# Performance work log

Hardware: AMD Instinct MI355X
Metric: run time of the kernel (lower is better)

## Reference

```python
import jax, jax.numpy as jnp
import numpy as np

B, S, D, H = 4, 127, 768, 12
HD = D // H
NS = S + 1
GAMMA = 1.0
NEG_INF = -1e9
EPS = 1e-6


def setup_inputs() -> dict:
    key = jax.random.key(0)
    ks = jax.random.split(key, 12)
    s = 0.02
    return {
        'desc': jax.random.normal(ks[0], (B, S, D), jnp.float32),
        'nve': jax.random.normal(ks[1], (B, NS, D), jnp.float32),
        'mask_M': jax.random.uniform(ks[2], (B, H, S, S), jnp.float32),
        'Wq': jax.random.normal(ks[3], (D, D), jnp.float32) * s,
        'bq': jnp.zeros((D,), jnp.float32),
        'Wk': jax.random.normal(ks[4], (D, D), jnp.float32) * s,
        'bk': jnp.zeros((D,), jnp.float32),
        'Wv': jax.random.normal(ks[5], (D, D), jnp.float32) * s,
        'bv': jnp.zeros((D,), jnp.float32),
        'eW1': jax.random.normal(ks[6], (2 * D, D), jnp.float32) * s,
        'eb1': jnp.zeros((D,), jnp.float32),
        'ln_g': jnp.ones((D,), jnp.float32),
        'ln_b': jnp.zeros((D,), jnp.float32),
        'eW2': jax.random.normal(ks[7], (D, D), jnp.float32) * s,
        'eb2': jnp.zeros((D,), jnp.float32),
        'aW': jax.random.normal(ks[8], (3 * HD,), jnp.float32) * s,
        'ab': jnp.zeros((), jnp.float32),
    }


def _layernorm(x, g, b):
    m = jnp.mean(x, -1, keepdims=True)
    v = jnp.var(x, -1, keepdims=True)
    return (x - m) * jax.lax.rsqrt(v + 1e-5) * g + b


def _adjacency():
    # CLS->Var on, Var->CLS off, Var-Var without self loop
    var_adj = 1.0 - jnp.eye(S, dtype=jnp.float32)
    adj = jnp.zeros((NS, NS), jnp.float32)
    adj = adj.at[1:, 1:].set(var_adj)
    adj = adj.at[0, 1:].set(1.0)
    return adj  # [NS, NS]


def reference(desc, nve, mask_M, Wq, bq, Wk, bk, Wv, bv, eW1, eb1, ln_g, ln_b, eW2, eb2, aW, ab):
    adj = _adjacency()

    def proj(W, bias):
        return (nve @ W + bias).reshape(B, NS, H, HD).transpose(0, 2, 1, 3)  # [B,H,NS,HD]

    q, k, v = proj(Wq, bq), proj(Wk, bk), proj(Wv, bv)

    # edge features: pairwise concat of desc embeddings, CLS edges = [desc, desc]
    node_i = jnp.broadcast_to(desc[:, :, None, :], (B, S, S, D))
    node_j = jnp.broadcast_to(desc[:, None, :, :], (B, S, S, D))
    var_edge = jnp.concatenate([node_i, node_j], -1)           # [B,S,S,2D]
    cls_edge = jnp.concatenate([desc, desc], -1)               # [B,S,2D]
    edge = jnp.zeros((B, NS, NS, 2 * D), jnp.float32)
    edge = edge.at[:, 1:, 1:].set(var_edge)
    edge = edge.at[:, 0, 1:].set(cls_edge)
    edge = edge.at[:, 1:, 0].set(cls_edge)

    # edge_update MLP: Linear -> LayerNorm -> ReLU -> Linear
    h = jax.nn.relu(_layernorm(edge @ eW1 + eb1, ln_g, ln_b))
    e = h @ eW2 + eb2                                           # [B,NS,NS,D]
    e = e.reshape(B, NS, NS, H, HD).transpose(0, 3, 1, 2, 4)    # [B,H,NS,NS,HD]
    e = e * adj[None, None, :, :, None]

    # attn_proj on concat([q_i, k_j, e_ij]) == sum of three dot products + bias
    aq, ak, ae = aW[:HD], aW[HD:2 * HD], aW[2 * HD:]
    logits = (jnp.einsum('bhid,d->bhi', q, aq)[:, :, :, None]
              + jnp.einsum('bhjd,d->bhj', k, ak)[:, :, None, :]
              + jnp.einsum('bhijd,d->bhij', e, ae) + ab)        # [B,H,NS,NS]

    # logit bias from Var-Var probabilities
    p = jnp.clip(mask_M, EPS, 1.0 - EPS)
    bias = (jnp.log(p) - jnp.log(1.0 - p)) * GAMMA
    logits = logits.at[:, :, 1:, 1:].add(bias)

    logits = logits + jnp.where(adj == 0.0, NEG_INF, 0.0)[None, None]
    attn = jax.nn.softmax(logits, axis=-1)                      # dropout off (eval)
    context = jnp.einsum('bhij,bhjd->bhid', attn, v)
    basis_outputs = context.transpose(0, 2, 1, 3)               # [B,NS,H,HD]
    return basis_outputs, attn
```

## Files before the change

### kernel.cpp

```cpp
#include <hip/hip_runtime.h>
#include <hip/hip_bf16.h>

#define BB  4
#define SS  127
#define DD  768
#define HH  12
#define HDl 64
#define NSl 128

typedef __attribute__((ext_vector_type(8))) short short8;
typedef __attribute__((ext_vector_type(4))) float f32x4;

constexpr int OFF_P   = 0;
constexpr int OFF_Q   = OFF_P  + BB*SS*DD;
constexpr int OFF_V   = OFF_Q  + BB*SS*DD;
constexpr int OFF_QA  = OFF_V  + BB*NSl*DD;
constexpr int OFF_KA  = OFF_QA + BB*NSl*HH;
constexpr int OFF_W2B = OFF_KA + BB*NSl*HH;
constexpr int OFF_WQA = OFF_W2B + 6144;
constexpr int OFF_WKA = OFF_WQA + HH*DD;
constexpr int OFF_BF  = OFF_WKA + HH*DD;
constexpr int OFF_SP  = OFF_BF + 64;
constexpr int OFF_SSP = OFF_SP + BB*128;
constexpr int OFF_SQ  = OFF_SSP + BB*128;
constexpr int OFF_SSQ = OFF_SQ + BB*128;
constexpr int OFF_EL  = OFF_SSQ + BB*128;

__device__ inline unsigned short f2bf(float f) {
    unsigned int u = __builtin_bit_cast(unsigned int, f);
    u += 0x7fffu + ((u >> 16) & 1u);
    return (unsigned short)(u >> 16);
}

__device__ inline short8 pack8(float4 a, float4 b) {
    short8 p;
    p[0] = (short)f2bf(a.x); p[1] = (short)f2bf(a.y);
    p[2] = (short)f2bf(a.z); p[3] = (short)f2bf(a.w);
    p[4] = (short)f2bf(b.x); p[5] = (short)f2bf(b.y);
    p[6] = (short)f2bf(b.z); p[7] = (short)f2bf(b.w);
    return p;
}

__device__ inline void unpack8(short8 s, float* f) {
    int4 u = __builtin_bit_cast(int4, s);
    f[0] = __builtin_bit_cast(float, u.x << 16);
    f[1] = __builtin_bit_cast(float, u.x & 0xffff0000);
    f[2] = __builtin_bit_cast(float, u.y << 16);
    f[3] = __builtin_bit_cast(float, u.y & 0xffff0000);
    f[4] = __builtin_bit_cast(float, u.z << 16);
    f[5] = __builtin_bit_cast(float, u.z & 0xffff0000);
    f[6] = __builtin_bit_cast(float, u.w << 16);
    f[7] = __builtin_bit_cast(float, u.w & 0xffff0000);
}

__device__ inline unsigned int cvtpk(float lo, float hi) {
    unsigned int r;
    asm volatile("v_cvt_pk_bf16_f32 %0, %1, %2" : "=v"(r) : "v"(lo), "v"(hi));
    return r;
}

constexpr int NB_PQ   = 96;
constexpr int NB_V    = 96;
constexpr int FOLD_T  = 3 * HH * DD + 36 + 4 * DD;
constexpr int NB_FOLD = (FOLD_T + 511) / 512;

__global__ __launch_bounds__(512) void mega1(
        const float* __restrict__ desc, const float* __restrict__ nve,
        const float* __restrict__ eW1, const float* __restrict__ Wv,
        const float* __restrict__ bv, const float* __restrict__ eb1,
        const float* __restrict__ Wq, const float* __restrict__ Wk,
        const float* __restrict__ eW2,
        const float* __restrict__ bq, const float* __restrict__ bk,
        const float* __restrict__ eb2, const float* __restrict__ aW,
        float* __restrict__ P, float* __restrict__ Qm, float* __restrict__ V,
        unsigned short* __restrict__ W2Bu, float* __restrict__ WQA,
        float* __restrict__ WKA, float* __restrict__ bfold) {
    const int bid = blockIdx.x;
    const int tid = threadIdx.x;

    if (bid >= NB_PQ + NB_V) {
        int idx = (bid - NB_PQ - NB_V) * 512 + tid;
        const int total = 3 * HH * DD;
        if (idx < total) {
            int which = idx / (HH * DD);
            int r = idx % (HH * DD);
            int h = r / DD;
            int c = r % DD;
            const float* W = (which == 0) ? eW2 : (which == 1) ? Wq : Wk;
            const float* a = (which == 0) ? (aW + 2 * HDl) : (which == 1) ? aW : (aW + HDl);
            float s = 0.f;
            #pragma unroll 8
            for (int d = 0; d < HDl; ++d) s += W[c * DD + h * HDl + d] * a[d];
            if (which == 0) W2Bu[h * DD + c] = f2bf(s);
            else if (which == 1) WQA[h * DD + c] = s;
            else WKA[h * DD + c] = s;
        } else if (idx < total + 36) {
            int r = idx - total;
            int which = r / HH, h = r % HH;
            const float* bb = (which == 0) ? eb2 : (which == 1) ? bq : bk;
            const float* a = (which == 0) ? (aW + 2 * HDl) : (which == 1) ? aW : (aW + HDl);
            float s = 0.f;
            for (int d = 0; d < HDl; ++d) s += bb[h * HDl + d] * a[d];
            bfold[r] = s;
        } else if (idx < FOLD_T) {
            W2Bu[12 * DD + (idx - total - 36)] = 0;
        }
        return;
    }

    const bool pq = (bid < NB_PQ);
    const int r = pq ? bid : bid - NB_PQ;
    const int bcol = (r % 12) * 64;
    const int brow = (r / 12) * 64;
    const float* A  = pq ? desc : nve;
    const float* B0 = pq ? eW1 : Wv;
    const int M = pq ? (BB * SS) : (BB * NSl);

    __shared__ short lds[3 * 64 * 64];
    short* As  = lds;
    short* Bs0 = lds + 4096;
    short* Bs1 = lds + 8192;

    const int arow = tid >> 3, akc = (tid & 7) * 8;
    const int abyte = (arow * 128 + akc * 2) ^ ((arow & 7) << 4);
    const int bn = tid & 63, bg = tid >> 6;
    const int bbyte = (bn * 128 + bg * 16) ^ ((bn & 7) << 4);

    const int gm = brow + arow;
    const float* arow_p = A + gm * DD + akc;

    short8 gA, gB0, gB1;
    auto loadA = [&](int k0) {
        float4 f0 = {0,0,0,0}, f1 = {0,0,0,0};
        if (gm < M) {
            f0 = *(const float4*)(arow_p + k0);
            f1 = *(const float4*)(arow_p + k0 + 4);
        }
        gA = pack8(f0, f1);
    };
    auto loadB = [&](const float* Bm, int k0, short8& dst) {
        float v[8];
        #pragma unroll
        for (int q = 0; q < 8; ++q)
            v[q] = Bm[(k0 + bg * 8 + q) * DD + bcol + bn];
        short8 p;
        #pragma unroll
        for (int q = 0; q < 8; ++q) p[q] = (short)f2bf(v[q]);
        dst = p;
    };

    loadA(0);
    loadB(B0, 0, gB0);
    if (pq) loadB(eW1 + DD * DD, 0, gB1);

    const int lane = tid & 63;
    const int w = tid >> 6;
    const int wr = w >> 1, wc = w & 1;
    const int l15 = lane & 15;

    f32x4 acc0[2] = {};
    f32x4 acc1[2] = {};

    for (int k0 = 0; k0 < DD; k0 += 64) {
        *(short8*)((char*)As + abyte) = gA;
        *(short8*)((char*)Bs0 + bbyte) = gB0;
        if (pq) *(short8*)((char*)Bs1 + bbyte) = gB1;
        __syncthreads();
        if (k0 + 64 < DD) {
            loadA(k0 + 64);
            loadB(B0, k0 + 64, gB0);
            if (pq) loadB(eW1 + DD * DD, k0 + 64, gB1);
        }
        #pragma unroll
        for (int ks = 0; ks < 2; ++ks) {
            const int kb = ks * 64 + ((lane >> 4) << 4);
            int row = wr * 16 + l15;
            short8 af = *(const short8*)((char*)As + ((row * 128 + kb) ^ ((row & 7) << 4)));
            #pragma unroll
            for (int ni = 0; ni < 2; ++ni) {
                int col = wc * 32 + ni * 16 + l15;
                int cb = (col * 128 + kb) ^ ((col & 7) << 4);
                short8 b0 = *(const short8*)((char*)Bs0 + cb);
                acc0[ni] = __builtin_amdgcn_mfma_f32_16x16x32_bf16(af, b0, acc0[ni], 0, 0, 0);
                if (pq) {
                    short8 b1 = *(const short8*)((char*)Bs1 + cb);
                    acc1[ni] = __builtin_amdgcn_mfma_f32_16x16x32_bf16(af, b1, acc1[ni], 0, 0, 0);
                }
            }
        }
        __syncthreads();
    }

    #pragma unroll
    for (int ni = 0; ni < 2; ++ni) {
        int gcol = bcol + wc * 32 + ni * 16 + l15;
        float bias0 = pq ? 0.f : bv[gcol];
        float bias1 = pq ? eb1[gcol] : 0.f;
        #pragma unroll
        for (int rr = 0; rr < 4; ++rr) {
            int grow = brow + wr * 16 + ((lane >> 4) << 2) + rr;
            if (grow < M) {
                if (pq) {
                    P[grow * DD + gcol]  = acc0[ni][rr];
                    Qm[grow * DD + gcol] = acc1[ni][rr] + bias1;
                } else {
                    V[grow * DD + gcol] = acc0[ni][rr] + bias0;
                }
            }
        }
    }
}

__global__ void statqk_kernel(const float* __restrict__ Pp, const float* __restrict__ Qp,
                              const float* __restrict__ nve,
                              const float* __restrict__ WQA, const float* __restrict__ WKA,
                              const float* __restrict__ bfold,
                              float* __restrict__ SP, float* __restrict__ SSP,
                              float* __restrict__ SQ, float* __restrict__ SSQ,
                              float* __restrict__ qa, float* __restrict__ ka) {
    int wid = blockIdx.x * 4 + (threadIdx.x >> 6);
    int lane = threadIdx.x & 63;
    const int NSTAT = BB * SS * 2;
    if (wid < NSTAT) {
        int which = wid & 1;
        int row = (wid >> 1) % SS;
        int b = (wid >> 1) / SS;
        const float* src = (which ? Qp : Pp) + (b * SS + row) * DD;
        float s = 0.f, ss = 0.f;
        #pragma unroll
        for (int r = 0; r < 12; ++r) {
            float v = src[lane + 64 * r];
            s += v;
            ss += v * v;
        }
        #pragma unroll
        for (int off = 32; off; off >>= 1) {
            s += __shfl_xor(s, off);
            ss += __shfl_xor(ss, off);
        }
        if (lane == 0) {
            (which ? SQ : SP)[b * 128 + row] = s;
            (which ? SSQ : SSP)[b * 128 + row] = ss;
        }
    } else {
        int t2 = wid - NSTAT;
        if (t2 >= BB * NSl * HH * 2) return;
        int which = t2 & 1;
        int r = t2 >> 1;
        int h = r % HH;
        int t = (r / HH) % NSl;
        int b = r / (HH * NSl);
        const float* W = (which ? WKA : WQA) + h * DD;
        const float* row = nve + (b * NSl + t) * DD;
        float s = 0.f;
        #pragma unroll
        for (int rr = 0; rr < 12; ++rr) {
            int c = lane + 64 * rr;
            s += row[c] * W[c];
        }
        #pragma unroll
        for (int off = 32; off; off >>= 1) s += __shfl_xor(s, off);
        if (lane == 0)
            (which ? ka : qa)[(b * NSl + t) * HH + h] = s + bfold[12 + which * 12 + h];
    }
}

__global__ __launch_bounds__(512) void pair_mfma(
        const float* __restrict__ Pp, const float* __restrict__ Qp,
        const float* __restrict__ ln_g, const float* __restrict__ ln_b,
        const unsigned short* __restrict__ W2Bu,
        const float* __restrict__ SP, const float* __restrict__ SSP,
        const float* __restrict__ SQ, const float* __restrict__ SSQ,
        const float* __restrict__ bfold,
        float* __restrict__ e_log) {
    __shared__ short pB[16 * 768];
    __shared__ short qB[16 * 768];
    __shared__ float gbl[2 * 768];

    const int b   = blockIdx.z;
    const int pi0 = blockIdx.y * 16, qj0 = blockIdx.x * 16;
    const int tid = threadIdx.x;

    {
        int row = tid >> 5;
        int ccb = tid & 31;
        const float* psrc = Pp + (b * SS + min(pi0 + row, SS - 1)) * DD;
        const float* qsrc = Qp + (b * SS + min(qj0 + row, SS - 1)) * DD;
        #pragma unroll
        for (int it = 0; it < 3; ++it) {
            int cc = ccb + it * 32;
            int byte = (row * 1536 + cc * 16) ^ ((row & 7) << 4);
            float4 a0 = *(const float4*)(psrc + cc * 8);
            float4 a1 = *(const float4*)(psrc + cc * 8 + 4);
            *(short8*)((char*)pB + byte) = pack8(a0, a1);
            a0 = *(const float4*)(qsrc + cc * 8);
            a1 = *(const float4*)(qsrc + cc * 8 + 4);
            *(short8*)((char*)qB + byte) = pack8(a0, a1);
        }
    }
    if (tid < 384) {
        int c = tid * 4;
        float4 v = (tid < 192) ? *(const float4*)(ln_g + c)
                               : *(const float4*)(ln_b + (c - 768));
        *(float4*)(gbl + c) = v;
    }
    __syncthreads();

    const int lane = tid & 63;
    const int w    = tid >> 6;
    const int l15  = lane & 15;
    const int kg   = lane >> 4;

    f32x4 gacc = {};
    #pragma unroll 4
    for (int ks = 0; ks < 24; ++ks) {
        int cb = ks * 64 + kg * 16;
        short8 ap = *(const short8*)((char*)pB + ((l15 * 1536 + cb) ^ ((l15 & 7) << 4)));
        short8 aq = *(const short8*)((char*)qB + ((l15 * 1536 + cb) ^ ((l15 & 7) << 4)));
        gacc = __builtin_amdgcn_mfma_f32_16x16x32_bf16(ap, aq, gacc, 0, 0, 0);
    }

    float al[2], be[2];
    #pragma unroll
    for (int s = 0; s < 2; ++s) {
        int pl = 2 * w + s;
        int src = ((pl >> 2) << 4) | l15;
        int rsel = pl & 3;
        float gg = (rsel == 0) ? gacc[0] : (rsel == 1) ? gacc[1]
                 : (rsel == 2) ? gacc[2] : gacc[3];
        gg = __shfl(gg, src);
        int pig = min(pi0 + pl, SS - 1);
        int qjg = min(qj0 + l15, SS - 1);
        float mean = (SP[b * 128 + pig] + SQ[b * 128 + qjg]) * (1.f / DD);
        float sumsq = SSP[b * 128 + pig] + 2.f * gg + SSQ[b * 128 + qjg];
        float var = sumsq * (1.f / DD) - mean * mean;
        float a = rsqrtf(var + 1e-5f);
        al[s] = a;
        be[s] = -mean * a;
    }

    const unsigned short* wrow = W2Bu + l15 * 768;
    const int r0 = 2 * w, r1 = 2 * w + 1;
    const int p0base = r0 * 1536, p1base = r1 * 1536;
    const int p0x = (r0 & 7) << 4, p1x = (r1 & 7) << 4;
    f32x4 acc0 = {}, acc1 = {};

    #pragma unroll 2
    for (int ks = 0; ks < 24; ++ks) {
        const int c0 = ks * 32 + kg * 8;
        short8 bfg = *(const short8*)(wrow + c0);
        f32x4 g0 = *(const f32x4*)(gbl + c0);
        f32x4 g1 = *(const f32x4*)(gbl + c0 + 4);
        f32x4 bb0 = *(const f32x4*)(gbl + 768 + c0);
        f32x4 bb1 = *(const f32x4*)(gbl + 768 + c0 + 4);
        float gv[8] = {g0.x, g0.y, g0.z, g0.w, g1.x, g1.y, g1.z, g1.w};
        float bv8[8] = {bb0.x, bb0.y, bb0.z, bb0.w, bb1.x, bb1.y, bb1.z, bb1.w};

        short8 q8 = *(const short8*)((char*)qB + ((l15 * 1536 + c0 * 2) ^ ((l15 & 7) << 4)));
        float qf[8];
        unpack8(q8, qf);

        short8 p8 = *(const short8*)((char*)pB + ((p0base + c0 * 2) ^ p0x));
        float pf[8];
        unpack8(p8, pf);
        float y[8];
        #pragma unroll
        for (int j = 0; j < 8; ++j) {
            float t = pf[j] + qf[j];
            float u = __builtin_fmaf(al[0], t, be[0]);
            y[j] = fmaxf(__builtin_fmaf(gv[j], u, bv8[j]), 0.f);
        }
        {
            int4 ti = { (int)cvtpk(y[0], y[1]), (int)cvtpk(y[2], y[3]),
                        (int)cvtpk(y[4], y[5]), (int)cvtpk(y[6], y[7]) };
            short8 ya = __builtin_bit_cast(short8, ti);
            acc0 = __builtin_amdgcn_mfma_f32_16x16x32_bf16(ya, bfg, acc0, 0, 0, 0);
        }

        p8 = *(const short8*)((char*)pB + ((p1base + c0 * 2) ^ p1x));
        unpack8(p8, pf);
        #pragma unroll
        for (int j = 0; j < 8; ++j) {
            float t = pf[j] + qf[j];
            float u = __builtin_fmaf(al[1], t, be[1]);
            y[j] = fmaxf(__builtin_fmaf(gv[j], u, bv8[j]), 0.f);
        }
        {
            int4 ti = { (int)cvtpk(y[0], y[1]), (int)cvtpk(y[2], y[3]),
                        (int)cvtpk(y[4], y[5]), (int)cvtpk(y[6], y[7]) };
            short8 ya = __builtin_bit_cast(short8, ti);
            acc1 = __builtin_amdgcn_mfma_f32_16x16x32_bf16(ya, bfg, acc1, 0, 0, 0);
        }
    }

    if (l15 < HH) {
        const float badd = bfold[l15];
        #pragma unroll
        for (int s = 0; s < 2; ++s) {
            int pig = pi0 + 2 * w + s;
            if (pig >= SS) continue;
            f32x4 A = s ? acc1 : acc0;
            #pragma unroll
            for (int r = 0; r < 4; ++r) {
                int qjg = qj0 + (kg << 2) + r;
                if (qjg < SS) {
                    int i = (pig == qjg) ? 0 : (pig + 1);
                    e_log[(((b * HH + l15) * NSl) + i) * NSl + (qjg + 1)] = A[r] + badd;
                }
            }
        }
    }
}

__global__ __launch_bounds__(512) void softmax_ctx_kernel(
        const float* __restrict__ e_log,
        const float* __restrict__ qa, const float* __restrict__ ka,
        const float* __restrict__ mask_M, const float* __restrict__ ab,
        const float* __restrict__ V,
        float* __restrict__ out) {
    __shared__ short Vt[64 * 128];
    __shared__ short plb[32 * 128];
    __shared__ float kal[NSl];

    const int b = blockIdx.z;
    const int h = blockIdx.y;
    const int iq = blockIdx.x;
    const int tid = threadIdx.x;
    const int lane = tid & 63;
    const int w = tid >> 6;

    {
        int j = tid >> 2;
        int dq = (tid & 3) * 16;
        const float* src = V + (b * NSl + j) * DD + h * HDl + dq;
        float4 f0 = *(const float4*)(src);
        float4 f1 = *(const float4*)(src + 4);
        float4 f2 = *(const float4*)(src + 8);
        float4 f3 = *(const float4*)(src + 12);
        float vv[16] = {f0.x,f0.y,f0.z,f0.w, f1.x,f1.y,f1.z,f1.w,
                        f2.x,f2.y,f2.z,f2.w, f3.x,f3.y,f3.z,f3.w};
        #pragma unroll
        for (int t = 0; t < 16; ++t) {
            int d = dq + t;
            int byte = (d * 256 + j * 2) ^ ((d & 7) << 4);
            *(short*)((char*)Vt + byte) = (short)f2bf(vv[t]);
        }
    }
    if (tid < NSl) kal[tid] = ka[(b * NSl + tid) * HH + h];
    __syncthreads();

    const float abv = ab[0];

    for (int rr = 0; rr < 4; ++rr) {
        const int il = w * 4 + rr;
        const int i = iq * 32 + il;
        const float qv = qa[(b * NSl + i) * HH + h];
        const float* e_row = e_log + (((b * HH + h) * NSl) + i) * NSl;

        float lg[2];
        bool valid[2];
        #pragma unroll
        for (int s = 0; s < 2; ++s) {
            int j = 1 + lane + 64 * s;
            bool v = (j < NSl) && !(i >= 1 && j == i);
            float l = -1e30f;
            if (v) {
                l = e_row[j] + qv + kal[j] + abv;
                if (i >= 1) {
                    float p = mask_M[((b * HH + h) * SS + (i - 1)) * SS + (j - 1)];
                    p = fminf(fmaxf(p, 1e-6f), 1.0f - 1e-6f);
                    l += __logf(p / (1.0f - p));
                }
            }
            lg[s] = l;
            valid[s] = v;
        }
        float m = fmaxf(lg[0], lg[1]);
        #pragma unroll
        for (int off = 32; off; off >>= 1) m = fmaxf(m, __shfl_xor(m, off));
        float e0 = valid[0] ? __expf(lg[0] - m) : 0.f;
        float e1 = valid[1] ? __expf(lg[1] - m) : 0.f;
        float s = e0 + e1;
        #pragma unroll
        for (int off = 32; off; off >>= 1) s += __shfl_xor(s, off);
        const float inv = 1.0f / s;

        const float p0 = e0 * inv, p1 = e1 * inv;

        float* attn_row = out + BB * NSl * HH * HDl + (((b * HH + h) * NSl) + i) * NSl;
        attn_row[1 + lane] = p0;
        if (65 + lane < NSl) attn_row[65 + lane] = p1;
        if (lane == 0) attn_row[0] = 0.f;

        {
            int byte0 = (il * 256 + (1 + lane) * 2) ^ ((il & 7) << 4);
            *(short*)((char*)plb + byte0) = (short)f2bf(p0);
            if (65 + lane < NSl) {
                int byte1 = (il * 256 + (65 + lane) * 2) ^ ((il & 7) << 4);
                *(short*)((char*)plb + byte1) = (short)f2bf(p1);
            }
            if (lane == 0) {
                int byteZ = (il * 256) ^ ((il & 7) << 4);
                *(short*)((char*)plb + byteZ) = 0;
            }
        }
    }
    __syncthreads();

    const int l15 = lane & 15;
    const int kg  = lane >> 4;
    const int itile = w >> 2, dtile = w & 3;
    const int arow  = itile * 16 + l15;
    const int bcold = dtile * 16 + l15;
    f32x4 acc = {};
    #pragma unroll
    for (int ks = 0; ks < 4; ++ks) {
        int kb = (ks * 32 + kg * 8) * 2;
        short8 af = *(const short8*)((char*)plb + ((arow * 256 + kb) ^ ((arow & 7) << 4)));
        short8 bf = *(const short8*)((char*)Vt  + ((bcold * 256 + kb) ^ ((bcold & 7) << 4)));
        acc = __builtin_amdgcn_mfma_f32_16x16x32_bf16(af, bf, acc, 0, 0, 0);
    }
    #pragma unroll
    for (int r = 0; r < 4; ++r) {
        int i = iq * 32 + itile * 16 + kg * 4 + r;
        out[((b * NSl + i) * HH + h) * HDl + dtile * 16 + l15] = acc[r];
    }
}

extern "C" void kernel_launch(void* const* d_in, const int* in_sizes, int n_in,
                              void* d_out, int out_size, void* d_ws, size_t ws_size,
                              hipStream_t stream) {
    const float* desc   = (const float*)d_in[0];
    const float* nve    = (const float*)d_in[1];
    const float* mask_M = (const float*)d_in[2];
    const float* Wq     = (const float*)d_in[3];
    const float* bq     = (const float*)d_in[4];
    const float* Wk     = (const float*)d_in[5];
    const float* bk     = (const float*)d_in[6];
    const float* Wv     = (const float*)d_in[7];
    const float* bv     = (const float*)d_in[8];
    const float* eW1    = (const float*)d_in[9];
    const float* eb1    = (const float*)d_in[10];
    const float* ln_g   = (const float*)d_in[11];
    const float* ln_b   = (const float*)d_in[12];
    const float* eW2    = (const float*)d_in[13];
    const float* eb2    = (const float*)d_in[14];
    const float* aW     = (const float*)d_in[15];
    const float* ab     = (const float*)d_in[16];

    float* ws  = (float*)d_ws;
    float* out = (float*)d_out;
    unsigned short* W2Bu = (unsigned short*)(ws + OFF_W2B);

    mega1<<<NB_PQ + NB_V + NB_FOLD, 512, 0, stream>>>(
        desc, nve, eW1, Wv, bv, eb1,
        Wq, Wk, eW2, bq, bk, eb2, aW,
        ws + OFF_P, ws + OFF_Q, ws + OFF_V,
        W2Bu, ws + OFF_WQA, ws + OFF_WKA, ws + OFF_BF);

    statqk_kernel<<<(BB * SS * 2 + BB * NSl * HH * 2 + 3) / 4, 256, 0, stream>>>(
        ws + OFF_P, ws + OFF_Q, nve, ws + OFF_WQA, ws + OFF_WKA, ws + OFF_BF,
        ws + OFF_SP, ws + OFF_SSP, ws + OFF_SQ, ws + OFF_SSQ,
        ws + OFF_QA, ws + OFF_KA);

    pair_mfma<<<dim3(8, 8, BB), 512, 0, stream>>>(
        ws + OFF_P, ws + OFF_Q, ln_g, ln_b, W2Bu,
        ws + OFF_SP, ws + OFF_SSP, ws + OFF_SQ, ws + OFF_SSQ,
        ws + OFF_BF, ws + OFF_EL);

    softmax_ctx_kernel<<<dim3(4, HH, BB), 512, 0, stream>>>(
        ws + OFF_EL, ws + OFF_QA, ws + OFF_KA, mask_M, ab, ws + OFF_V, out);
}
```

Measured before the change: 57.55 us.

## Fuse row-stat and qa/ka kernel into pair MFMA kernel

Removes the separate statqk kernel. The per-row sum and sum-of-squares of P and Q are now computed inside the pair kernel while it stages those rows into shared memory, so no global stat buffers are needed. The qa/ka attention-projection dot products run as extra blocks on the same grid, appended along z. This drops one launch and a global round trip, in exchange for some redundant stat work per tile and a larger, mixed-role grid.

```diff
diff --git a/kernel.cpp b/kernel.cpp
--- a/kernel.cpp
+++ b/kernel.cpp
@@ -20,11 +20,7 @@
 constexpr int OFF_WQA = OFF_W2B + 6144;
 constexpr int OFF_WKA = OFF_WQA + HH*DD;
 constexpr int OFF_BF  = OFF_WKA + HH*DD;
-constexpr int OFF_SP  = OFF_BF + 64;
-constexpr int OFF_SSP = OFF_SP + BB*128;
-constexpr int OFF_SQ  = OFF_SSP + BB*128;
-constexpr int OFF_SSQ = OFF_SQ + BB*128;
-constexpr int OFF_EL  = OFF_SSQ + BB*128;
+constexpr int OFF_EL  = OFF_BF + 64;
 
 __device__ inline unsigned short f2bf(float f) {
     unsigned int u = __builtin_bit_cast(unsigned int, f);
@@ -211,42 +207,29 @@
     }
 }
 
-__global__ void statqk_kernel(const float* __restrict__ Pp, const float* __restrict__ Qp,
-                              const float* __restrict__ nve,
-                              const float* __restrict__ WQA, const float* __restrict__ WKA,
-                              const float* __restrict__ bfold,
-                              float* __restrict__ SP, float* __restrict__ SSP,
-                              float* __restrict__ SQ, float* __restrict__ SSQ,
-                              float* __restrict__ qa, float* __restrict__ ka) {
-    int wid = blockIdx.x * 4 + (threadIdx.x >> 6);
-    int lane = threadIdx.x & 63;
-    const int NSTAT = BB * SS * 2;
-    if (wid < NSTAT) {
+__global__ __launch_bounds__(512) void pairqk_kernel(
+        const float* __restrict__ Pp, const float* __restrict__ Qp,
+        const float* __restrict__ nve,
+        const float* __restrict__ ln_g, const float* __restrict__ ln_b,
+        const unsigned short* __restrict__ W2Bu,
+        const float* __restrict__ WQA, const float* __restrict__ WKA,
+        const float* __restrict__ bfold,
+        float* __restrict__ qa, float* __restrict__ ka,
+        float* __restrict__ e_log) {
+    __shared__ short pB[16 * 768];
+    __shared__ short qB[16 * 768];
+    __shared__ float gbl[2 * 768];
+    __shared__ float2 pstat[16];
+    __shared__ float2 qstat[16];
+
+    const int tid = threadIdx.x;
+
+    if (blockIdx.z >= BB) {
+        int qb = (blockIdx.z - BB) * 64 + blockIdx.y * 8 + blockIdx.x;
+        int wid = qb * 8 + (tid >> 6);
+        int lane = tid & 63;
         int which = wid & 1;
-        int row = (wid >> 1) % SS;
-        int b = (wid >> 1) / SS;
-        const float* src = (which ? Qp : Pp) + (b * SS + row) * DD;
-        float s = 0.f, ss = 0.f;
-        #pragma unroll
-        for (int r = 0; r < 12; ++r) {
-            float v = src[lane + 64 * r];
-            s += v;
-            ss += v * v;
-        }
-        #pragma unroll
-        for (int off = 32; off; off >>= 1) {
-            s += __shfl_xor(s, off);
-            ss += __shfl_xor(ss, off);
-        }
-        if (lane == 0) {
-            (which ? SQ : SP)[b * 128 + row] = s;
-            (which ? SSQ : SSP)[b * 128 + row] = ss;
-        }
-    } else {
-        int t2 = wid - NSTAT;
-        if (t2 >= BB * NSl * HH * 2) return;
-        int which = t2 & 1;
-        int r = t2 >> 1;
+        int r = wid >> 1;
         int h = r % HH;
         int t = (r / HH) % NSl;
         int b = r / (HH * NSl);
@@ -262,40 +245,45 @@
         for (int off = 32; off; off >>= 1) s += __shfl_xor(s, off);
         if (lane == 0)
             (which ? ka : qa)[(b * NSl + t) * HH + h] = s + bfold[12 + which * 12 + h];
-    }
-}
-
-__global__ __launch_bounds__(512) void pair_mfma(
-        const float* __restrict__ Pp, const float* __restrict__ Qp,
-        const float* __restrict__ ln_g, const float* __restrict__ ln_b,
-        const unsigned short* __restrict__ W2Bu,
-        const float* __restrict__ SP, const float* __restrict__ SSP,
-        const float* __restrict__ SQ, const float* __restrict__ SSQ,
-        const float* __restrict__ bfold,
-        float* __restrict__ e_log) {
-    __shared__ short pB[16 * 768];
-    __shared__ short qB[16 * 768];
-    __shared__ float gbl[2 * 768];
+        return;
+    }
 
     const int b   = blockIdx.z;
     const int pi0 = blockIdx.y * 16, qj0 = blockIdx.x * 16;
-    const int tid = threadIdx.x;
 
     {
         int row = tid >> 5;
         int ccb = tid & 31;
         const float* psrc = Pp + (b * SS + min(pi0 + row, SS - 1)) * DD;
         const float* qsrc = Qp + (b * SS + min(qj0 + row, SS - 1)) * DD;
+        float ps = 0.f, pss = 0.f, qs = 0.f, qss = 0.f;
         #pragma unroll
         for (int it = 0; it < 3; ++it) {
             int cc = ccb + it * 32;
             int byte = (row * 1536 + cc * 16) ^ ((row & 7) << 4);
             float4 a0 = *(const float4*)(psrc + cc * 8);
             float4 a1 = *(const float4*)(psrc + cc * 8 + 4);
+            ps  += (a0.x + a0.y + a0.z + a0.w) + (a1.x + a1.y + a1.z + a1.w);
+            pss += a0.x*a0.x + a0.y*a0.y + a0.z*a0.z + a0.w*a0.w
+                 + a1.x*a1.x + a1.y*a1.y + a1.z*a1.z + a1.w*a1.w;
             *(short8*)((char*)pB + byte) = pack8(a0, a1);
             a0 = *(const float4*)(qsrc + cc * 8);
             a1 = *(const float4*)(qsrc + cc * 8 + 4);
+            qs  += (a0.x + a0.y + a0.z + a0.w) + (a1.x + a1.y + a1.z + a1.w);
+            qss += a0.x*a0.x + a0.y*a0.y + a0.z*a0.z + a0.w*a0.w
+                 + a1.x*a1.x + a1.y*a1.y + a1.z*a1.z + a1.w*a1.w;
             *(short8*)((char*)qB + byte) = pack8(a0, a1);
+        }
+        #pragma unroll
+        for (int off = 16; off; off >>= 1) {
+            ps  += __shfl_xor(ps, off);
+            pss += __shfl_xor(pss, off);
+            qs  += __shfl_xor(qs, off);
+            qss += __shfl_xor(qss, off);
+        }
+        if ((tid & 31) == 0) {
+            pstat[tid >> 5] = make_float2(ps, pss);
+            qstat[tid >> 5] = make_float2(qs, qss);
         }
     }
     if (tid < 384) {
@@ -329,10 +317,10 @@
         float gg = (rsel == 0) ? gacc[0] : (rsel == 1) ? gacc[1]
                  : (rsel == 2) ? gacc[2] : gacc[3];
         gg = __shfl(gg, src);
-        int pig = min(pi0 + pl, SS - 1);
-        int qjg = min(qj0 + l15, SS - 1);
-        float mean = (SP[b * 128 + pig] + SQ[b * 128 + qjg]) * (1.f / DD);
-        float sumsq = SSP[b * 128 + pig] + 2.f * gg + SSQ[b * 128 + qjg];
+        float2 pst = pstat[pl];
+        float2 qst = qstat[l15];
+        float mean = (pst.x + qst.x) * (1.f / DD);
+        float sumsq = pst.y + 2.f * gg + qst.y;
         float var = sumsq * (1.f / DD) - mean * mean;
         float a = rsqrtf(var + 1e-5f);
         al[s] = a;
@@ -558,15 +546,10 @@
         ws + OFF_P, ws + OFF_Q, ws + OFF_V,
         W2Bu, ws + OFF_WQA, ws + OFF_WKA, ws + OFF_BF);
 
-    statqk_kernel<<<(BB * SS * 2 + BB * NSl * HH * 2 + 3) / 4, 256, 0, stream>>>(
-        ws + OFF_P, ws + OFF_Q, nve, ws + OFF_WQA, ws + OFF_WKA, ws + OFF_BF,
-        ws + OFF_SP, ws + OFF_SSP, ws + OFF_SQ, ws + OFF_SSQ,
-        ws + OFF_QA, ws + OFF_KA);
-
-    pair_mfma<<<dim3(8, 8, BB), 512, 0, stream>>>(
-        ws + OFF_P, ws + OFF_Q, ln_g, ln_b, W2Bu,
-        ws + OFF_SP, ws + OFF_SSP, ws + OFF_SQ, ws + OFF_SSQ,
-        ws + OFF_BF, ws + OFF_EL);
+    pairqk_kernel<<<dim3(8, 8, BB + 24), 512, 0, stream>>>(
+        ws + OFF_P, ws + OFF_Q, nve, ln_g, ln_b, W2Bu,
+        ws + OFF_WQA, ws + OFF_WKA, ws + OFF_BF,
+        ws + OFF_QA, ws + OFF_KA, ws + OFF_EL);
 
     softmax_ctx_kernel<<<dim3(4, HH, BB), 512, 0, stream>>>(
         ws + OFF_EL, ws + OFF_QA, ws + OFF_KA, mask_M, ab, ws + OFF_V, out);
```

New measurement: 54.55 us. 5.2% less time.
